# Kernel optimization log

Measured on AMD Instinct MI355X. Metric: run time of the kernel, lower is better.

## Reference

```python
import jax, jax.numpy as jnp
import numpy as np

N_NODES = 100000
N_EDGES = 1600000
IN_FEATS = 128
HIDDEN = 128
NUM_CLASSES = 4


def setup_inputs() -> dict:
    key = jax.random.key(0)
    ks = jax.random.split(key, 8)
    features = jax.random.normal(ks[0], (N_NODES, IN_FEATS), dtype=jnp.float32)
    src = jax.random.randint(ks[1], (N_EDGES,), 0, N_NODES, dtype=jnp.int64)
    dst = jax.random.randint(ks[2], (N_EDGES,), 0, N_NODES, dtype=jnp.int64)
    s = 1.0 / np.sqrt(IN_FEATS)
    W1 = jax.random.normal(ks[3], (IN_FEATS, HIDDEN), dtype=jnp.float32) * s
    b1 = jnp.zeros((HIDDEN,), dtype=jnp.float32)
    W2 = jax.random.normal(ks[4], (HIDDEN, HIDDEN), dtype=jnp.float32) * s
    b2 = jnp.zeros((HIDDEN,), dtype=jnp.float32)
    Wc = jax.random.normal(ks[5], (HIDDEN, NUM_CLASSES), dtype=jnp.float32) * s
    bc = jnp.zeros((NUM_CLASSES,), dtype=jnp.float32)
    return {"features": features, "src": src, "dst": dst,
            "W1": W1, "b1": b1, "W2": W2, "b2": b2, "Wc": Wc, "bc": bc}


def _graph_conv(x, W, b, src, dst, n_nodes, activation=True):
    # DGL GraphConv, norm='both': D_out^{-1/2} A^T D_in... i.e. symmetric norm.
    ones = jnp.ones((src.shape[0],), dtype=x.dtype)
    deg_out = jnp.clip(jax.ops.segment_sum(ones, src, num_segments=n_nodes), 1.0)
    deg_in = jnp.clip(jax.ops.segment_sum(ones, dst, num_segments=n_nodes), 1.0)
    # scale sources, project (in >= out so matmul first, math-equivalent), gather-scatter
    h = (x * (deg_out ** -0.5)[:, None]) @ W            # [N, out]
    msg = h[src]                                         # [E, out] gather
    agg = jax.ops.segment_sum(msg, dst, num_segments=n_nodes)  # [N, out] scatter-add
    h = agg * (deg_in ** -0.5)[:, None] + b
    return jax.nn.relu(h) if activation else h


def reference(features, src, dst, W1, b1, W2, b2, Wc, bc):
    # eval-mode forward: dropout is identity
    n = features.shape[0]
    h = _graph_conv(features, W1, b1, src, dst, n, activation=True)
    h = _graph_conv(h, W2, b2, src, dst, n, activation=True)
    return h @ Wc + bc  # [N, num_classes] logits
```

## Files before the change

kernel.cpp:

```cpp
#include <hip/hip_runtime.h>
#include <hip/hip_fp16.h>
#include <math.h>

#define N_NODES 100000
#define N_EDGES 1600000
#define F 128
#define NBUK 196
#define BSH 9
#define BSZ 512
#define CAP 9216

typedef _Float16 half8 __attribute__((ext_vector_type(8)));
typedef float    f32x4 __attribute__((ext_vector_type(4)));

__global__ __launch_bounds__(256) void init_csr(int* __restrict__ curD,
                                                int* __restrict__ curS,
                                                _Float16* __restrict__ padrow)
{
    int t = threadIdx.x;
    if (t < NBUK) { curD[t] = t * CAP; curS[t] = t * CAP; }
    if (t < 16) reinterpret_cast<int4*>(padrow)[t] = make_int4(0, 0, 0, 0);
}

__global__ __launch_bounds__(512) void partition(const int* __restrict__ src,
                                                 const int* __restrict__ dst,
                                                 int* __restrict__ curD,
                                                 int* __restrict__ curS,
                                                 int* __restrict__ bukD,
                                                 int* __restrict__ bukS)
{
    __shared__ int hd[NBUK], hs[NBUK], bd[NBUK], bs[NBUK], cd[NBUK], cs[NBUK];
    const int tid = threadIdx.x;
    const int chunk = (((N_EDGES + NBUK - 1) / NBUK) + 3) & ~3;
    const int beg = blockIdx.x * chunk;
    const int end = min(beg + chunk, N_EDGES);
    if (beg >= end) return;
    if (tid < NBUK) { hd[tid] = 0; hs[tid] = 0; cd[tid] = 0; cs[tid] = 0; }
    __syncthreads();
    const int b4 = beg >> 2, e4 = end >> 2;
    for (int i = b4 + tid; i < e4; i += 512) {
        int4 d = reinterpret_cast<const int4*>(dst)[i];
        int4 s = reinterpret_cast<const int4*>(src)[i];
        atomicAdd(&hd[d.x >> BSH], 1); atomicAdd(&hd[d.y >> BSH], 1);
        atomicAdd(&hd[d.z >> BSH], 1); atomicAdd(&hd[d.w >> BSH], 1);
        atomicAdd(&hs[s.x >> BSH], 1); atomicAdd(&hs[s.y >> BSH], 1);
        atomicAdd(&hs[s.z >> BSH], 1); atomicAdd(&hs[s.w >> BSH], 1);
    }
    __syncthreads();
    if (tid < NBUK) {
        bd[tid] = hd[tid] ? atomicAdd(&curD[tid], hd[tid]) : 0;
        bs[tid] = hs[tid] ? atomicAdd(&curS[tid], hs[tid]) : 0;
    }
    __syncthreads();
    for (int e = beg + tid; e < end; e += 512) {
        int d = dst[e], s = src[e];
        int bin = d >> BSH;
        int r = atomicAdd(&cd[bin], 1);
        bukD[bd[bin] + r] = ((d & 511) << 17) | s;
        int bin2 = s >> BSH;
        int r2 = atomicAdd(&cs[bin2], 1);
        bukS[bs[bin2] + r2] = s;
    }
}

__global__ __launch_bounds__(512) void csr_bucket(const int* __restrict__ bukD,
                                                  const int* __restrict__ curD,
                                                  int* __restrict__ row_ptr,
                                                  float* __restrict__ sin_,
                                                  int* __restrict__ col)
{
    __shared__ int h[BSZ], sc[BSZ], cur[BSZ];
    const int tid = threadIdx.x;
    const int n0 = blockIdx.x << BSH;
    const int lo = blockIdx.x * CAP, hi = curD[blockIdx.x];
    h[tid] = 0;
    __syncthreads();
    for (int i = lo + tid; i < hi; i += 512)
        atomicAdd(&h[((unsigned)bukD[i]) >> 17], 1);
    __syncthreads();
    int own = h[tid];
    sc[tid] = own;
    __syncthreads();
    for (int off = 1; off < 512; off <<= 1) {
        int u = (tid >= off) ? sc[tid - off] : 0;
        __syncthreads();
        sc[tid] += u;
        __syncthreads();
    }
    int ex = sc[tid] - own;
    cur[tid] = ex;
    int node = n0 + tid;
    if (node < N_NODES) {
        row_ptr[2 * node]     = lo + ex;
        row_ptr[2 * node + 1] = lo + ex + own;
        sin_[node] = rsqrtf((float)max(own, 1));
    }
    __syncthreads();
    for (int i = lo + tid; i < hi; i += 512) {
        int p = bukD[i];
        int r = atomicAdd(&cur[((unsigned)p) >> 17], 1);
        col[lo + r] = p & 0x1FFFF;
    }
}

__global__ __launch_bounds__(512) void deg_bucket(const int* __restrict__ bukS,
                                                  const int* __restrict__ curS,
                                                  float* __restrict__ sout)
{
    __shared__ int h[BSZ];
    const int tid = threadIdx.x;
    const int n0 = blockIdx.x << BSH;
    const int lo = blockIdx.x * CAP, hi = curS[blockIdx.x];
    h[tid] = 0;
    __syncthreads();
    for (int i = lo + tid; i < hi; i += 512)
        atomicAdd(&h[bukS[i] - n0], 1);
    __syncthreads();
    int node = n0 + tid;
    if (node < N_NODES) sout[node] = rsqrtf((float)max(h[tid], 1));
}

__global__ __launch_bounds__(256) void pack_w2(const float* __restrict__ W1,
                                               const float* __restrict__ W2,
                                               _Float16* __restrict__ hi1,
                                               _Float16* __restrict__ lo1,
                                               _Float16* __restrict__ hi2,
                                               _Float16* __restrict__ lo2)
{
    int gidx = blockIdx.x * 256 + threadIdx.x;
    if (gidx >= 32768) return;
    const float* W = (gidx < 16384) ? W1 : W2;
    _Float16* hi = (gidx < 16384) ? hi1 : hi2;
    _Float16* lo = (gidx < 16384) ? lo1 : lo2;
    int idx = gidx & 16383;
    int f = idx >> 9, r = idx & 511;
    int l = r >> 3, j = r & 7;
    int kc = f >> 3, ct = f & 7;
    int k = kc * 32 + (l >> 4) * 8 + j;
    int n = ct * 16 + (l & 15);
    float w = W[k * 128 + n];
    _Float16 h = (_Float16)w;
    hi[idx] = h;
    lo[idx] = (_Float16)(w - (float)h);
}

__global__ __launch_bounds__(256) void gemm_mfma_f32(const float* __restrict__ X,
                                                     const _Float16* __restrict__ Whi,
                                                     const _Float16* __restrict__ Wlo,
                                                     const float* __restrict__ srow,
                                                     _Float16* __restrict__ Y, int N)
{
    const int tid = threadIdx.x;
    const int l = tid & 63, w = tid >> 6;
    const int quad = l >> 4, m = l & 15;
    const int row0 = blockIdx.x * 128;
    const half8* Bh = reinterpret_cast<const half8*>(Whi);
    const half8* Bl = reinterpret_cast<const half8*>(Wlo);

    f32x4 acc[2][8] = {};

    for (int kc = 0; kc < 4; kc++) {
        half8 ah[2], al[2];
        #pragma unroll
        for (int rt = 0; rt < 2; rt++) {
            int grow = row0 + w * 32 + rt * 16 + m;
            float4 xa = make_float4(0.f, 0.f, 0.f, 0.f), xb = xa;
            if (grow < N) {
                const float4* Xp = reinterpret_cast<const float4*>(X) + (size_t)grow * 32 + kc * 8 + quad * 2;
                xa = Xp[0]; xb = Xp[1];
            }
            float xs[8] = {xa.x, xa.y, xa.z, xa.w, xb.x, xb.y, xb.z, xb.w};
            #pragma unroll
            for (int j = 0; j < 8; j++) {
                _Float16 h = (_Float16)xs[j];
                ah[rt][j] = h;
                al[rt][j] = (_Float16)(xs[j] - (float)h);
            }
        }
        #pragma unroll
        for (int ct = 0; ct < 8; ct++) {
            int f = kc * 8 + ct;
            half8 bh = Bh[f * 64 + l];
            half8 bl = Bl[f * 64 + l];
            #pragma unroll
            for (int rt = 0; rt < 2; rt++) {
                acc[rt][ct] = __builtin_amdgcn_mfma_f32_16x16x32_f16(ah[rt], bh, acc[rt][ct], 0, 0, 0);
                acc[rt][ct] = __builtin_amdgcn_mfma_f32_16x16x32_f16(al[rt], bh, acc[rt][ct], 0, 0, 0);
                acc[rt][ct] = __builtin_amdgcn_mfma_f32_16x16x32_f16(ah[rt], bl, acc[rt][ct], 0, 0, 0);
            }
        }
    }

    #pragma unroll
    for (int rt = 0; rt < 2; rt++) {
        #pragma unroll
        for (int r = 0; r < 4; r++) {
            int grow = row0 + w * 32 + rt * 16 + quad * 4 + r;
            if (grow < N) {
                float s = srow[grow];
                #pragma unroll
                for (int ct = 0; ct < 8; ct++)
                    Y[(size_t)grow * 128 + ct * 16 + m] = (_Float16)(acc[rt][ct][r] * s);
            }
        }
    }
}

__global__ __launch_bounds__(256) void gemm_mfma_f16(const _Float16* __restrict__ Xh,
                                                     const _Float16* __restrict__ Whi,
                                                     const _Float16* __restrict__ Wlo,
                                                     const float* __restrict__ srow,
                                                     _Float16* __restrict__ Y, int N)
{
    const int tid = threadIdx.x;
    const int l = tid & 63, w = tid >> 6;
    const int quad = l >> 4, m = l & 15;
    const int row0 = blockIdx.x * 128;
    const half8* Bh = reinterpret_cast<const half8*>(Whi);
    const half8* Bl = reinterpret_cast<const half8*>(Wlo);

    f32x4 acc[2][8] = {};

    for (int kc = 0; kc < 4; kc++) {
        half8 a[2];
        #pragma unroll
        for (int rt = 0; rt < 2; rt++) {
            int grow = row0 + w * 32 + rt * 16 + m;
            half8 z = {};
            a[rt] = (grow < N)
                ? *reinterpret_cast<const half8*>(Xh + (size_t)grow * 128 + kc * 32 + quad * 8)
                : z;
        }
        #pragma unroll
        for (int ct = 0; ct < 8; ct++) {
            int f = kc * 8 + ct;
            half8 bh = Bh[f * 64 + l];
            half8 bl = Bl[f * 64 + l];
            #pragma unroll
            for (int rt = 0; rt < 2; rt++) {
                acc[rt][ct] = __builtin_amdgcn_mfma_f32_16x16x32_f16(a[rt], bh, acc[rt][ct], 0, 0, 0);
                acc[rt][ct] = __builtin_amdgcn_mfma_f32_16x16x32_f16(a[rt], bl, acc[rt][ct], 0, 0, 0);
            }
        }
    }

    #pragma unroll
    for (int rt = 0; rt < 2; rt++) {
        #pragma unroll
        for (int r = 0; r < 4; r++) {
            int grow = row0 + w * 32 + rt * 16 + quad * 4 + r;
            if (grow < N) {
                float s = srow[grow];
                #pragma unroll
                for (int ct = 0; ct < 8; ct++)
                    Y[(size_t)grow * 128 + ct * 16 + m] = (_Float16)(acc[rt][ct][r] * s);
            }
        }
    }
}

__global__ __launch_bounds__(256) void gather_agg(const __half* __restrict__ Hh,
                                                  const int* __restrict__ row_ptr,
                                                  const int* __restrict__ col,
                                                  const float* __restrict__ sin_,
                                                  const float* __restrict__ bias,
                                                  __half* __restrict__ Yh, int N)
{
    int node = blockIdx.x * 4 + (threadIdx.x >> 6);
    if (node >= N) return;
    int lane = threadIdx.x & 63;
    int beg = row_ptr[2 * node], end = row_ptr[2 * node + 1];
    const __half2* H2 = reinterpret_cast<const __half2*>(Hh);
    float2 acc0 = make_float2(0.f, 0.f);
    float2 acc1 = make_float2(0.f, 0.f);
    int i = beg;
    for (; i + 3 < end; i += 4) {
        int s0 = col[i], s1 = col[i + 1], s2 = col[i + 2], s3 = col[i + 3];
        __half2 v0 = H2[((size_t)s0 << 6) | lane];
        __half2 v1 = H2[((size_t)s1 << 6) | lane];
        __half2 v2 = H2[((size_t)s2 << 6) | lane];
        __half2 v3 = H2[((size_t)s3 << 6) | lane];
        float2 f0 = __half22float2(v0), f1 = __half22float2(v1);
        float2 f2 = __half22float2(v2), f3 = __half22float2(v3);
        acc0.x += f0.x + f1.x; acc0.y += f0.y + f1.y;
        acc1.x += f2.x + f3.x; acc1.y += f2.y + f3.y;
    }
    for (; i < end; i++) {
        int s = col[i];
        float2 f = __half22float2(H2[((size_t)s << 6) | lane]);
        acc0.x += f.x; acc0.y += f.y;
    }
    float sc = sin_[node];
    float2 b = reinterpret_cast<const float2*>(bias)[lane];
    float ox = fmaxf((acc0.x + acc1.x) * sc + b.x, 0.f);
    float oy = fmaxf((acc0.y + acc1.y) * sc + b.y, 0.f);
    reinterpret_cast<__half2*>(Yh)[((size_t)node << 6) | lane] = __floats2half2_rn(ox, oy);
}

__global__ __launch_bounds__(256) void classifier(const __half* __restrict__ Hh,
                                                  const float* __restrict__ Wc,
                                                  const float* __restrict__ bc,
                                                  float* __restrict__ out, int N)
{
    __shared__ float4 Wcs[128];
    for (int i = threadIdx.x; i < 128; i += 256)
        Wcs[i] = reinterpret_cast<const float4*>(Wc)[i];
    __syncthreads();
    int i = blockIdx.x * 256 + threadIdx.x;
    if (i < N) {
        float4 acc = reinterpret_cast<const float4*>(bc)[0];
        const __half2* h2 = reinterpret_cast<const __half2*>(Hh) + (size_t)i * 64;
        #pragma unroll
        for (int j = 0; j < 64; j++) {
            float2 f = __half22float2(h2[j]);
            float4 w0 = Wcs[2 * j], w1 = Wcs[2 * j + 1];
            acc.x += f.x * w0.x + f.y * w1.x;
            acc.y += f.x * w0.y + f.y * w1.y;
            acc.z += f.x * w0.z + f.y * w1.z;
            acc.w += f.x * w0.w + f.y * w1.w;
        }
        reinterpret_cast<float4*>(out)[i] = acc;
    }
}

extern "C" void kernel_launch(void* const* d_in, const int* in_sizes, int n_in,
                              void* d_out, int out_size, void* d_ws, size_t ws_size,
                              hipStream_t stream)
{
    const float* features = (const float*)d_in[0];
    const int*   src      = (const int*)d_in[1];
    const int*   dst      = (const int*)d_in[2];
    const float* W1       = (const float*)d_in[3];
    const float* b1       = (const float*)d_in[4];
    const float* W2       = (const float*)d_in[5];
    const float* b2       = (const float*)d_in[6];
    const float* Wc       = (const float*)d_in[7];
    const float* bc       = (const float*)d_in[8];
    float* out = (float*)d_out;

    char* ws = (char*)d_ws;
    const size_t MB = 1 << 20;
    int* curD  = (int*)(ws + 0);
    int* curS  = (int*)(ws + 1024);
    float* sout    = (float*)(ws + 1 * MB);
    float* sin_    = (float*)(ws + 2 * MB);
    int*   row_ptr = (int*)(ws + 3 * MB);
    int*   col     = (int*)(ws + 4 * MB);
    int*   bukD    = (int*)(ws + 12 * MB);
    int*   bukS    = (int*)(ws + 20 * MB);
    _Float16* Whi1 = (_Float16*)(ws + 28 * MB);
    _Float16* Wlo1 = (_Float16*)(ws + 28 * MB + 32 * 1024);
    _Float16* Whi2 = (_Float16*)(ws + 28 * MB + 64 * 1024);
    _Float16* Wlo2 = (_Float16*)(ws + 28 * MB + 96 * 1024);
    _Float16* hMsg = (_Float16*)(ws + 29 * MB);
    _Float16* hA   = (_Float16*)(ws + 55 * MB);

    const int N = N_NODES;
    const int GBLK = (N + 127) / 128;

    init_csr<<<1, 256, 0, stream>>>(curD, curS, hMsg + (size_t)N * F);
    partition<<<NBUK, 512, 0, stream>>>(src, dst, curD, curS, bukD, bukS);
    csr_bucket<<<NBUK, 512, 0, stream>>>(bukD, curD, row_ptr, sin_, col);
    deg_bucket<<<NBUK, 512, 0, stream>>>(bukS, curS, sout);

    pack_w2<<<128, 256, 0, stream>>>(W1, W2, Whi1, Wlo1, Whi2, Wlo2);

    gemm_mfma_f32<<<GBLK, 256, 0, stream>>>(features, Whi1, Wlo1, sout, hMsg, N);
    gather_agg<<<(N + 3) / 4, 256, 0, stream>>>((const __half*)hMsg, row_ptr, col, sin_, b1, (__half*)hA, N);

    gemm_mfma_f16<<<GBLK, 256, 0, stream>>>(hA, Whi2, Wlo2, sout, hMsg, N);
    gather_agg<<<(N + 3) / 4, 256, 0, stream>>>((const __half*)hMsg, row_ptr, col, sin_, b2, (__half*)hA, N);

    classifier<<<(N + 255) / 256, 256, 0, stream>>>((const __half*)hA, Wc, bc, out, N);
}
```

Baseline: 354.9 us.

## Fuse partition with first GEMM and merge CSR/degree kernels

Merges init and weight packing into one launch, runs edge partitioning and the first-layer GEMM in one heterogeneous grid (GEMM now 256 rows per 512-thread block, no out-degree scaling), and merges the CSR build and out-degree kernels. Because sout is no longer ready when the first GEMM runs, the source-degree scaling moves into a new gather kernel that loads sout per edge. This removes launches and lets the GEMM overlap the partition work, at the cost of an extra per-edge scalar gather in the first aggregation.

Measured after the change: 343.4 us. 1.03x faster.

```diff
diff --git a/kernel.cpp b/kernel.cpp
--- a/kernel.cpp
+++ b/kernel.cpp
@@ -13,122 +13,23 @@
 typedef _Float16 half8 __attribute__((ext_vector_type(8)));
 typedef float    f32x4 __attribute__((ext_vector_type(4)));
 
-__global__ __launch_bounds__(256) void init_csr(int* __restrict__ curD,
-                                                int* __restrict__ curS,
-                                                _Float16* __restrict__ padrow)
+__global__ __launch_bounds__(256) void init_pack(int* __restrict__ curD,
+                                                 int* __restrict__ curS,
+                                                 _Float16* __restrict__ padrow,
+                                                 const float* __restrict__ W1,
+                                                 const float* __restrict__ W2,
+                                                 _Float16* __restrict__ hi1,
+                                                 _Float16* __restrict__ lo1,
+                                                 _Float16* __restrict__ hi2,
+                                                 _Float16* __restrict__ lo2)
 {
     int t = threadIdx.x;
-    if (t < NBUK) { curD[t] = t * CAP; curS[t] = t * CAP; }
-    if (t < 16) reinterpret_cast<int4*>(padrow)[t] = make_int4(0, 0, 0, 0);
-}
-
-__global__ __launch_bounds__(512) void partition(const int* __restrict__ src,
-                                                 const int* __restrict__ dst,
-                                                 int* __restrict__ curD,
-                                                 int* __restrict__ curS,
-                                                 int* __restrict__ bukD,
-                                                 int* __restrict__ bukS)
-{
-    __shared__ int hd[NBUK], hs[NBUK], bd[NBUK], bs[NBUK], cd[NBUK], cs[NBUK];
-    const int tid = threadIdx.x;
-    const int chunk = (((N_EDGES + NBUK - 1) / NBUK) + 3) & ~3;
-    const int beg = blockIdx.x * chunk;
-    const int end = min(beg + chunk, N_EDGES);
-    if (beg >= end) return;
-    if (tid < NBUK) { hd[tid] = 0; hs[tid] = 0; cd[tid] = 0; cs[tid] = 0; }
-    __syncthreads();
-    const int b4 = beg >> 2, e4 = end >> 2;
-    for (int i = b4 + tid; i < e4; i += 512) {
-        int4 d = reinterpret_cast<const int4*>(dst)[i];
-        int4 s = reinterpret_cast<const int4*>(src)[i];
-        atomicAdd(&hd[d.x >> BSH], 1); atomicAdd(&hd[d.y >> BSH], 1);
-        atomicAdd(&hd[d.z >> BSH], 1); atomicAdd(&hd[d.w >> BSH], 1);
-        atomicAdd(&hs[s.x >> BSH], 1); atomicAdd(&hs[s.y >> BSH], 1);
-        atomicAdd(&hs[s.z >> BSH], 1); atomicAdd(&hs[s.w >> BSH], 1);
-    }
-    __syncthreads();
-    if (tid < NBUK) {
-        bd[tid] = hd[tid] ? atomicAdd(&curD[tid], hd[tid]) : 0;
-        bs[tid] = hs[tid] ? atomicAdd(&curS[tid], hs[tid]) : 0;
-    }
-    __syncthreads();
-    for (int e = beg + tid; e < end; e += 512) {
-        int d = dst[e], s = src[e];
-        int bin = d >> BSH;
-        int r = atomicAdd(&cd[bin], 1);
-        bukD[bd[bin] + r] = ((d & 511) << 17) | s;
-        int bin2 = s >> BSH;
-        int r2 = atomicAdd(&cs[bin2], 1);
-        bukS[bs[bin2] + r2] = s;
-    }
-}
-
-__global__ __launch_bounds__(512) void csr_bucket(const int* __restrict__ bukD,
-                                                  const int* __restrict__ curD,
-                                                  int* __restrict__ row_ptr,
-                                                  float* __restrict__ sin_,
-                                                  int* __restrict__ col)
-{
-    __shared__ int h[BSZ], sc[BSZ], cur[BSZ];
-    const int tid = threadIdx.x;
-    const int n0 = blockIdx.x << BSH;
-    const int lo = blockIdx.x * CAP, hi = curD[blockIdx.x];
-    h[tid] = 0;
-    __syncthreads();
-    for (int i = lo + tid; i < hi; i += 512)
-        atomicAdd(&h[((unsigned)bukD[i]) >> 17], 1);
-    __syncthreads();
-    int own = h[tid];
-    sc[tid] = own;
-    __syncthreads();
-    for (int off = 1; off < 512; off <<= 1) {
-        int u = (tid >= off) ? sc[tid - off] : 0;
-        __syncthreads();
-        sc[tid] += u;
-        __syncthreads();
-    }
-    int ex = sc[tid] - own;
-    cur[tid] = ex;
-    int node = n0 + tid;
-    if (node < N_NODES) {
-        row_ptr[2 * node]     = lo + ex;
-        row_ptr[2 * node + 1] = lo + ex + own;
-        sin_[node] = rsqrtf((float)max(own, 1));
-    }
-    __syncthreads();
-    for (int i = lo + tid; i < hi; i += 512) {
-        int p = bukD[i];
-        int r = atomicAdd(&cur[((unsigned)p) >> 17], 1);
-        col[lo + r] = p & 0x1FFFF;
-    }
-}
-
-__global__ __launch_bounds__(512) void deg_bucket(const int* __restrict__ bukS,
-                                                  const int* __restrict__ curS,
-                                                  float* __restrict__ sout)
-{
-    __shared__ int h[BSZ];
-    const int tid = threadIdx.x;
-    const int n0 = blockIdx.x << BSH;
-    const int lo = blockIdx.x * CAP, hi = curS[blockIdx.x];
-    h[tid] = 0;
-    __syncthreads();
-    for (int i = lo + tid; i < hi; i += 512)
-        atomicAdd(&h[bukS[i] - n0], 1);
-    __syncthreads();
-    int node = n0 + tid;
-    if (node < N_NODES) sout[node] = rsqrtf((float)max(h[tid], 1));
-}
-
-__global__ __launch_bounds__(256) void pack_w2(const float* __restrict__ W1,
-                                               const float* __restrict__ W2,
-                                               _Float16* __restrict__ hi1,
-                                               _Float16* __restrict__ lo1,
-                                               _Float16* __restrict__ hi2,
-                                               _Float16* __restrict__ lo2)
-{
-    int gidx = blockIdx.x * 256 + threadIdx.x;
-    if (gidx >= 32768) return;
+    if (blockIdx.x == 0) {
+        if (t < NBUK) { curD[t] = t * CAP; curS[t] = t * CAP; }
+        if (t < 16) reinterpret_cast<int4*>(padrow)[t] = make_int4(0, 0, 0, 0);
+        return;
+    }
+    int gidx = (blockIdx.x - 1) * 256 + t;
     const float* W = (gidx < 16384) ? W1 : W2;
     _Float16* hi = (gidx < 16384) ? hi1 : hi2;
     _Float16* lo = (gidx < 16384) ? lo1 : lo2;
@@ -144,16 +45,57 @@
     lo[idx] = (_Float16)(w - (float)h);
 }
 
-__global__ __launch_bounds__(256) void gemm_mfma_f32(const float* __restrict__ X,
-                                                     const _Float16* __restrict__ Whi,
-                                                     const _Float16* __restrict__ Wlo,
-                                                     const float* __restrict__ srow,
-                                                     _Float16* __restrict__ Y, int N)
-{
+__global__ __launch_bounds__(512) void part_gemm1(const int* __restrict__ src,
+                                                  const int* __restrict__ dst,
+                                                  int* __restrict__ curD,
+                                                  int* __restrict__ curS,
+                                                  int* __restrict__ bukD,
+                                                  int* __restrict__ bukS,
+                                                  const float* __restrict__ X,
+                                                  const _Float16* __restrict__ Whi,
+                                                  const _Float16* __restrict__ Wlo,
+                                                  _Float16* __restrict__ Y, int N)
+{
+    __shared__ int hd[NBUK], hs[NBUK], bd[NBUK], bs[NBUK], cd[NBUK], cs[NBUK];
     const int tid = threadIdx.x;
+
+    if (blockIdx.x < NBUK) {
+        const int chunk = (((N_EDGES + NBUK - 1) / NBUK) + 3) & ~3;
+        const int beg = blockIdx.x * chunk;
+        const int end = min(beg + chunk, N_EDGES);
+        if (beg >= end) return;
+        if (tid < NBUK) { hd[tid] = 0; hs[tid] = 0; cd[tid] = 0; cs[tid] = 0; }
+        __syncthreads();
+        const int b4 = beg >> 2, e4 = end >> 2;
+        for (int i = b4 + tid; i < e4; i += 512) {
+            int4 d = reinterpret_cast<const int4*>(dst)[i];
+            int4 s = reinterpret_cast<const int4*>(src)[i];
+            atomicAdd(&hd[d.x >> BSH], 1); atomicAdd(&hd[d.y >> BSH], 1);
+            atomicAdd(&hd[d.z >> BSH], 1); atomicAdd(&hd[d.w >> BSH], 1);
+            atomicAdd(&hs[s.x >> BSH], 1); atomicAdd(&hs[s.y >> BSH], 1);
+            atomicAdd(&hs[s.z >> BSH], 1); atomicAdd(&hs[s.w >> BSH], 1);
+        }
+        __syncthreads();
+        if (tid < NBUK) {
+            bd[tid] = hd[tid] ? atomicAdd(&curD[tid], hd[tid]) : 0;
+            bs[tid] = hs[tid] ? atomicAdd(&curS[tid], hs[tid]) : 0;
+        }
+        __syncthreads();
+        for (int e = beg + tid; e < end; e += 512) {
+            int d = dst[e], s = src[e];
+            int bin = d >> BSH;
+            int r = atomicAdd(&cd[bin], 1);
+            bukD[bd[bin] + r] = ((d & 511) << 17) | s;
+            int bin2 = s >> BSH;
+            int r2 = atomicAdd(&cs[bin2], 1);
+            bukS[bs[bin2] + r2] = s;
+        }
+        return;
+    }
+
     const int l = tid & 63, w = tid >> 6;
     const int quad = l >> 4, m = l & 15;
-    const int row0 = blockIdx.x * 128;
+    const int row0 = (blockIdx.x - NBUK) * 256;
     const half8* Bh = reinterpret_cast<const half8*>(Whi);
     const half8* Bl = reinterpret_cast<const half8*>(Wlo);
 
@@ -197,13 +139,114 @@
         for (int r = 0; r < 4; r++) {
             int grow = row0 + w * 32 + rt * 16 + quad * 4 + r;
             if (grow < N) {
-                float s = srow[grow];
                 #pragma unroll
                 for (int ct = 0; ct < 8; ct++)
-                    Y[(size_t)grow * 128 + ct * 16 + m] = (_Float16)(acc[rt][ct][r] * s);
-            }
-        }
-    }
+                    Y[(size_t)grow * 128 + ct * 16 + m] = (_Float16)(acc[rt][ct][r]);
+            }
+        }
+    }
+}
+
+__global__ __launch_bounds__(512) void csr_deg(const int* __restrict__ bukD,
+                                               const int* __restrict__ bukS,
+                                               const int* __restrict__ curD,
+                                               const int* __restrict__ curS,
+                                               int* __restrict__ row_ptr,
+                                               float* __restrict__ sin_,
+                                               float* __restrict__ sout,
+                                               int* __restrict__ col)
+{
+    __shared__ int h[BSZ], sc[BSZ], cur[BSZ];
+    const int tid = threadIdx.x;
+
+    if (blockIdx.x >= NBUK) {
+        const int bid = blockIdx.x - NBUK;
+        const int n0 = bid << BSH;
+        const int lo = bid * CAP, hi = curS[bid];
+        h[tid] = 0;
+        __syncthreads();
+        for (int i = lo + tid; i < hi; i += 512)
+            atomicAdd(&h[bukS[i] - n0], 1);
+        __syncthreads();
+        int node = n0 + tid;
+        if (node < N_NODES) sout[node] = rsqrtf((float)max(h[tid], 1));
+        return;
+    }
+
+    const int n0 = blockIdx.x << BSH;
+    const int lo = blockIdx.x * CAP, hi = curD[blockIdx.x];
+    h[tid] = 0;
+    __syncthreads();
+    for (int i = lo + tid; i < hi; i += 512)
+        atomicAdd(&h[((unsigned)bukD[i]) >> 17], 1);
+    __syncthreads();
+    int own = h[tid];
+    sc[tid] = own;
+    __syncthreads();
+    for (int off = 1; off < 512; off <<= 1) {
+        int u = (tid >= off) ? sc[tid - off] : 0;
+        __syncthreads();
+        sc[tid] += u;
+        __syncthreads();
+    }
+    int ex = sc[tid] - own;
+    cur[tid] = ex;
+    int node = n0 + tid;
+    if (node < N_NODES) {
+        row_ptr[2 * node]     = lo + ex;
+        row_ptr[2 * node + 1] = lo + ex + own;
+        sin_[node] = rsqrtf((float)max(own, 1));
+    }
+    __syncthreads();
+    for (int i = lo + tid; i < hi; i += 512) {
+        int p = bukD[i];
+        int r = atomicAdd(&cur[((unsigned)p) >> 17], 1);
+        col[lo + r] = p & 0x1FFFF;
+    }
+}
+
+__global__ __launch_bounds__(256) void gather_agg_s(const __half* __restrict__ Hh,
+                                                    const int* __restrict__ row_ptr,
+                                                    const int* __restrict__ col,
+                                                    const float* __restrict__ sout,
+                                                    const float* __restrict__ sin_,
+                                                    const float* __restrict__ bias,
+                                                    __half* __restrict__ Yh, int N)
+{
+    int node = blockIdx.x * 4 + (threadIdx.x >> 6);
+    if (node >= N) return;
+    int lane = threadIdx.x & 63;
+    int beg = row_ptr[2 * node], end = row_ptr[2 * node + 1];
+    const __half2* H2 = reinterpret_cast<const __half2*>(Hh);
+    float2 acc0 = make_float2(0.f, 0.f);
+    float2 acc1 = make_float2(0.f, 0.f);
+    int i = beg;
+    for (; i + 3 < end; i += 4) {
+        int s0 = col[i], s1 = col[i + 1], s2 = col[i + 2], s3 = col[i + 3];
+        float w0 = sout[s0], w1 = sout[s1], w2 = sout[s2], w3 = sout[s3];
+        __half2 v0 = H2[((size_t)s0 << 6) | lane];
+        __half2 v1 = H2[((size_t)s1 << 6) | lane];
+        __half2 v2 = H2[((size_t)s2 << 6) | lane];
+        __half2 v3 = H2[((size_t)s3 << 6) | lane];
+        float2 f0 = __half22float2(v0), f1 = __half22float2(v1);
+        float2 f2 = __half22float2(v2), f3 = __half22float2(v3);
+        acc0.x = fmaf(w0, f0.x, fmaf(w1, f1.x, acc0.x));
+        acc0.y = fmaf(w0, f0.y, fmaf(w1, f1.y, acc0.y));
+        acc1.x = fmaf(w2, f2.x, fmaf(w3, f3.x, acc1.x));
+        acc1.y = fmaf(w2, f2.y, fmaf(w3, f3.y, acc1.y));
+    }
+    for (; i < end; i++) {
+        int s = col[i];
+        float w = sout[s];
+        float2 f = __half22float2(H2[((size_t)s << 6) | lane]);
+        acc0.x = fmaf(w, f.x, acc0.x);
+        acc0.y = fmaf(w, f.y, acc0.y);
+    }
+    float sc = sin_[node];
+    float2 b = reinterpret_cast<const float2*>(bias)[lane];
+    float ox = fmaxf((acc0.x + acc1.x) * sc + b.x, 0.f);
+    float oy = fmaxf((acc0.y + acc1.y) * sc + b.y, 0.f);
+    reinterpret_cast<__half2*>(Yh)[((size_t)node << 6) | lane] = __floats2half2_rn(ox, oy);
 }
 
 __global__ __launch_bounds__(256) void gemm_mfma_f16(const _Float16* __restrict__ Xh,
@@ -356,20 +399,22 @@
     _Float16* hA   = (_Float16*)(ws + 55 * MB);
 
     const int N = N_NODES;
-    const int GBLK = (N + 127) / 128;
-
-    init_csr<<<1, 256, 0, stream>>>(curD, curS, hMsg + (size_t)N * F);
-    partition<<<NBUK, 512, 0, stream>>>(src, dst, curD, curS, bukD, bukS);
-    csr_bucket<<<NBUK, 512, 0, stream>>>(bukD, curD, row_ptr, sin_, col);
-    deg_bucket<<<NBUK, 512, 0, stream>>>(bukS, curS, sout);
-
-    pack_w2<<<128, 256, 0, stream>>>(W1, W2, Whi1, Wlo1, Whi2, Wlo2);
-
-    gemm_mfma_f32<<<GBLK, 256, 0, stream>>>(features, Whi1, Wlo1, sout, hMsg, N);
-    gather_agg<<<(N + 3) / 4, 256, 0, stream>>>((const __half*)hMsg, row_ptr, col, sin_, b1, (__half*)hA, N);
-
-    gemm_mfma_f16<<<GBLK, 256, 0, stream>>>(hA, Whi2, Wlo2, sout, hMsg, N);
-    gather_agg<<<(N + 3) / 4, 256, 0, stream>>>((const __half*)hMsg, row_ptr, col, sin_, b2, (__half*)hA, N);
+
+    init_pack<<<129, 256, 0, stream>>>(curD, curS, hMsg + (size_t)N * F,
+                                       W1, W2, Whi1, Wlo1, Whi2, Wlo2);
+
+    part_gemm1<<<NBUK + 391, 512, 0, stream>>>(src, dst, curD, curS, bukD, bukS,
+                                               features, Whi1, Wlo1, hMsg, N);
+
+    csr_deg<<<2 * NBUK, 512, 0, stream>>>(bukD, bukS, curD, curS,
+                                          row_ptr, sin_, sout, col);
+
+    gather_agg_s<<<(N + 3) / 4, 256, 0, stream>>>((const __half*)hMsg, row_ptr, col,
+                                                  sout, sin_, b1, (__half*)hA, N);
+
+    gemm_mfma_f16<<<(N + 127) / 128, 256, 0, stream>>>(hA, Whi2, Wlo2, sout, hMsg, N);
+    gather_agg<<<(N + 3) / 4, 256, 0, stream>>>((const __half*)hMsg, row_ptr, col,
+                                                sin_, b2, (__half*)hA, N);
 
     classifier<<<(N + 255) / 256, 256, 0, stream>>>((const __half*)hA, Wc, bc, out, N);
 }
```
